# Kernel optimization log

Hardware: AMD Instinct MI355X
Metric: run time of the kernel (lower is better)

The kernel has to match this reference:

```python
import jax, jax.numpy as jnp
import numpy as np

B, S, H, D = 2, 2048, 16, 64  # batch, seq, heads, head_dim


def setup_inputs() -> dict:
    key = jax.random.key(0)
    kq, kk, kv = jax.random.split(key, 3)
    query = jax.random.normal(kq, (B, S, H, D), dtype=jnp.float32)
    key_l = jax.random.normal(kk, (B, S, H, D), dtype=jnp.float32)
    value = jax.random.normal(kv, (B, S, H, D), dtype=jnp.float32)
    # padding mask: all tokens valid
    attention_mask = jnp.ones((B, S), dtype=bool)
    # causal lower-triangular mask [1,1,S,S]
    causal_mask = jnp.tril(jnp.ones((S, S), dtype=bool))[None, None, :, :]
    return {"query": query, "key": key_l, "value": value,
            "attention_mask": attention_mask, "causal_mask": causal_mask}


def reference(query, key, value, attention_mask, causal_mask):
    b = query.shape[0]
    # broadcast causal mask to batch: (B,1,S,S)
    cm = jnp.broadcast_to(causal_mask, (b,) + causal_mask.shape[1:])
    # padding mask (B,S) -> (B,1,1,S), combine with causal
    am = attention_mask[:, None, None, :]
    mask = jnp.logical_and(cm, am)
    neg = jnp.finfo(query.dtype).min
    bias = jnp.where(mask, jnp.zeros((), query.dtype), jnp.full((), neg, query.dtype))
    sm_scale = 1.0 / jnp.sqrt(jnp.asarray(query.shape[-1], jnp.float32))
    # scores: (B,H,Sq,Sk)
    scores = jnp.einsum("bqhd,bkhd->bhqk", query, key) * sm_scale + bias
    # attention_softmax_in_fp32 = True
    probs = jax.nn.softmax(scores.astype(jnp.float32), axis=-1).astype(query.dtype)
    ctx = jnp.einsum("bhqk,bkhd->bqhd", probs, value)
    # merge heads -> hidden_size_per_partition
    return ctx.reshape(ctx.shape[0], ctx.shape[1], -1)
```

## Files before the change

kernel.cpp:

```cpp
#include <hip/hip_runtime.h>
#include <hip/hip_bf16.h>


typedef __attribute__((ext_vector_type(8))) short short8;
typedef __attribute__((ext_vector_type(4))) short short4v;
typedef __attribute__((ext_vector_type(4))) float f32x4;

__device__ __forceinline__ unsigned cvtpk(float a, float b) {
    __hip_bfloat162 h = __float22bfloat162_rn(make_float2(a, b));
    union { __hip_bfloat162 h; unsigned u; } c; c.h = h;
    return c.u;
}

__device__ __forceinline__ short8 pack8(float4 a, float4 b) {
    union { short8 s; unsigned u[4]; } w;
    w.u[0] = cvtpk(a.x, a.y); w.u[1] = cvtpk(a.z, a.w);
    w.u[2] = cvtpk(b.x, b.y); w.u[3] = cvtpk(b.z, b.w);
    return w.s;
}

__device__ __forceinline__ unsigned short f2b(float v) {
    union { __hip_bfloat16 h; unsigned short u; } c;
    c.h = __float2bfloat16(v);
    return c.u;
}

__device__ __forceinline__ float b2f(unsigned short u) {
    union { unsigned u; float f; } v; v.u = ((unsigned)u) << 16;
    return v.f;
}

#define TR64(dst, addr) \
    asm volatile("ds_read_b64_tr_b16 %0, %1" : "=v"(dst) : "v"(addr))

#define GLOAD_LDS16(g, l) \
    __builtin_amdgcn_global_load_lds((const __attribute__((address_space(1))) void*)(g), \
                                     (__attribute__((address_space(3))) void*)(l), 16, 0, 0)

__constant__ unsigned char JOBS[48][3] = {
    {31,0,16},{31,16,32},{30,15,31},{15,0,16},
    {30,0,15},{29,0,15},{29,15,30},{28,14,29},{14,0,15},
    {28,0,14},{27,0,14},{27,14,28},{26,13,27},{13,0,14},
    {26,0,13},{25,0,13},{25,13,26},{24,12,25},{12,0,13},
    {24,0,12},{23,0,12},{23,12,24},{22,11,23},{11,0,12},
    {22,0,11},{21,0,11},{21,11,22},{20,10,21},{10,0,11},
    {20,0,10},{19,0,10},{19,10,20},{18,9,19},{9,0,10},
    {18,0,9},{17,0,9},{17,9,18},{16,8,17},{8,0,9},
    {16,0,8},{7,0,8},
    {6,0,7},{5,0,6},{4,0,5},{3,0,4},{2,0,3},{1,0,2},{0,0,1}
};

__global__ __launch_bounds__(256, 4)
void CoreAttention_68710886801875_prepass(const float* __restrict__ K,
                                          const float* __restrict__ V,
                                          unsigned short* __restrict__ Kbf,
                                          unsigned short* __restrict__ Vbf)
{
    const int tile = blockIdx.x;
    const int bh = tile >> 5, kt = tile & 31;
    const size_t base = (size_t)(bh >> 4) * (2048 * 1024) + (size_t)(bh & 15) * 64;
    unsigned short* ktile = Kbf + (size_t)tile * 4096;
    unsigned short* vtile = Vbf + (size_t)tile * 4096;

#pragma unroll
    for (int it = 0; it < 2; ++it) {
        const int c = threadIdx.x + it * 256;
        {
            const int r  = c >> 3;
            const int c8 = (c & 7) ^ (r & 7);
            const float* src = K + base + (size_t)(kt * 64 + r) * 1024 + c8 * 8;
            *(short8*)(ktile + c * 8) = pack8(*(const float4*)src, *(const float4*)(src + 4));
        }
        {
            const int s = c >> 3, k_lo = (c >> 1) & 3, half = c & 1;
            const int k  = (s >> 2) * 4 + k_lo;
            const int c8 = (s & 3) * 2 + half;
            const float* src = V + base + (size_t)(kt * 64 + k) * 1024 + c8 * 8;
            *(short8*)(vtile + c * 8) = pack8(*(const float4*)src, *(const float4*)(src + 4));
        }
    }
}

template <int PRE>
__global__ __launch_bounds__(256, 4)
void CoreAttention_68710886801875_kernel(const float* __restrict__ Q,
                                         const float* __restrict__ K,
                                         const float* __restrict__ V,
                                         const unsigned short* __restrict__ Kbf,
                                         const unsigned short* __restrict__ Vbf,
                                         float* __restrict__ O,
                                         unsigned short* __restrict__ Opart,
                                         float* __restrict__ Lpart)
{
    constexpr int S = 2048, HD = 1024;
    constexpr float SCALE = 0.125f * 1.44269504088896340736f;

    __shared__ __align__(16) unsigned short ldsK[2][64 * 64];
    __shared__ __align__(16) unsigned short ldsV[2][64 * 64];
    __shared__ __align__(16) unsigned short ldsPT[4][64 * 16];

    const int tid = threadIdx.x;
    const int wid = tid >> 6, lane = tid & 63, g = lane >> 4, lm = lane & 15;

    const int bx     = blockIdx.x;
    const int r_     = bx >> 3;
    const int jobIdx = r_ >> 2;
    const int bh     = (bx & 7) * 4 + (r_ & 3);
    const int qt     = JOBS[jobIdx][0];
    const int t0     = JOBS[jobIdx][1];
    const int t1     = JOBS[jobIdx][2];
    const int b      = bh >> 4, h = bh & 15;
    const int q0     = qt << 6;
    const size_t base = ((size_t)b * S) * HD + (size_t)h * 64;

    const int r0 = tid >> 3, c8 = tid & 7;
    const float* kp0 = K + base + (size_t)r0 * HD + c8 * 8;
    const float* vp0 = V + base + (size_t)r0 * HD + c8 * 8;
    float4 kst[4], vst[4];
    const unsigned short* kbfB = Kbf + (size_t)bh * 32 * 4096;
    const unsigned short* vbfB = Vbf + (size_t)bh * 32 * 4096;

    auto STAGE_ISSUE = [&](int kt2, int buf) {
        if constexpr (PRE) {
            const unsigned short* ks = kbfB + (size_t)kt2 * 4096 + tid * 8;
            const unsigned short* vs = vbfB + (size_t)kt2 * 4096 + tid * 8;
            GLOAD_LDS16(ks,        &ldsK[buf][tid * 8]);
            GLOAD_LDS16(ks + 2048, &ldsK[buf][tid * 8 + 2048]);
            GLOAD_LDS16(vs,        &ldsV[buf][tid * 8]);
            GLOAD_LDS16(vs + 2048, &ldsV[buf][tid * 8 + 2048]);
        } else {
            const float* kp = kp0 + (size_t)kt2 * 64 * HD;
            const float* vp = vp0 + (size_t)kt2 * 64 * HD;
            kst[0] = *(const float4*)kp;
            kst[1] = *(const float4*)(kp + 4);
            kst[2] = *(const float4*)(kp + (size_t)32 * HD);
            kst[3] = *(const float4*)(kp + (size_t)32 * HD + 4);
            vst[0] = *(const float4*)vp;
            vst[1] = *(const float4*)(vp + 4);
            vst[2] = *(const float4*)(vp + (size_t)32 * HD);
            vst[3] = *(const float4*)(vp + (size_t)32 * HD + 4);
        }
    };
    auto STAGE_WRITE = [&](int buf) {
        if constexpr (!PRE) {
#pragma unroll
            for (int it = 0; it < 2; ++it) {
                const int r = r0 + it * 32;
                const unsigned byteK = (unsigned)((r * 128 + c8 * 16) ^ ((r & 7) << 4));
                *(short8*)((char*)&ldsK[buf][0] + byteK) = pack8(kst[it * 2], kst[it * 2 + 1]);
                const unsigned byteV = (unsigned)(((r >> 2) * 4 + (c8 >> 1)) * 128 +
                                                  (r & 3) * 32 + (c8 & 1) * 16);
                *(short8*)((char*)&ldsV[buf][0] + byteV) = pack8(vst[it * 2], vst[it * 2 + 1]);
            }
        }
    };

    short8 qf[2];
    {
        const float* qp = Q + base + (size_t)(q0 + wid * 16 + lm) * HD + g * 8;
#pragma unroll
        for (int ks = 0; ks < 2; ++ks) {
            float4 a = *(const float4*)(qp + ks * 32);
            float4 cc = *(const float4*)(qp + ks * 32 + 4);
            a.x *= SCALE; a.y *= SCALE; a.z *= SCALE; a.w *= SCALE;
            cc.x *= SCALE; cc.y *= SCALE; cc.z *= SCALE; cc.w *= SCALE;
            qf[ks] = pack8(a, cc);
        }
    }

    short8 ones;
#pragma unroll
    for (int j = 0; j < 8; ++j) ones[j] = (short)0x3F80;

    f32x4 oacc[4], lacc;
#pragma unroll
    for (int n = 0; n < 4; ++n) oacc[n] = (f32x4){0.f, 0.f, 0.f, 0.f};
    lacc = (f32x4){0.f, 0.f, 0.f, 0.f};

    const unsigned vBase = (unsigned)(size_t)&ldsV[0][0];
    const unsigned ptAddr = (unsigned)(size_t)&ldsPT[wid][0];

    STAGE_ISSUE(t0, 0);
    STAGE_WRITE(0);
    __syncthreads();

    for (int t = t0; t < t1; ++t) {
        const int cur = (t - t0) & 1;
        if (t + 1 < t1) STAGE_ISSUE(t + 1, cur ^ 1);

        const bool diag = (t == qt);
        const int nmax = diag ? wid : 3;

        f32x4 sv[4];
        __builtin_amdgcn_s_setprio(1);
#pragma unroll
        for (int n = 0; n < 4; ++n) {
            if (n <= nmax) {
                const int kr = n * 16 + lm;
                const unsigned b0 = cur * 8192u +
                    (unsigned)((kr * 128 + g * 16) ^ ((kr & 7) << 4));
                const unsigned b1 = cur * 8192u +
                    (unsigned)((kr * 128 + 64 + g * 16) ^ ((kr & 7) << 4));
                const short8 kf0 = *(const short8*)((const char*)&ldsK[0][0] + b0);
                const short8 kf1 = *(const short8*)((const char*)&ldsK[0][0] + b1);
                f32x4 acc = (f32x4){0.f, 0.f, 0.f, 0.f};
                acc = __builtin_amdgcn_mfma_f32_16x16x32_bf16(qf[0], kf0, acc, 0, 0, 0);
                acc = __builtin_amdgcn_mfma_f32_16x16x32_bf16(qf[1], kf1, acc, 0, 0, 0);
                if (diag && n == wid) {
#pragma unroll
                    for (int r = 0; r < 4; ++r)
                        if (lm > g * 4 + r) acc[r] = -1e30f;
                }
                sv[n] = acc;
            } else {
                sv[n] = (f32x4){-1e30f, -1e30f, -1e30f, -1e30f};
            }
        }
        __builtin_amdgcn_s_setprio(0);

#pragma unroll
        for (int n = 0; n < 4; ++n) {
            float p[4];
#pragma unroll
            for (int r = 0; r < 4; ++r) p[r] = exp2f(sv[n][r]);
            union { short4v s; unsigned uu[2]; } pk;
            pk.uu[0] = cvtpk(p[0], p[1]);
            pk.uu[1] = cvtpk(p[2], p[3]);
            const unsigned byte = (unsigned)((n * 4 + (lm >> 2)) * 128 +
                                             (lm & 3) * 32 + g * 8);
            *(short4v*)((char*)&ldsPT[wid][0] + byte) = pk.s;
        }

        asm volatile("s_waitcnt lgkmcnt(0)" ::: "memory");
        short4v vlo[2][4], vhi[2][4], pL[2], pH[2];
#pragma unroll
        for (int ks = 0; ks < 2; ++ks) {
            const unsigned sub = (unsigned)(8 * ks + 2 * g);
#pragma unroll
            for (int n = 0; n < 4; ++n) {
                const unsigned va = vBase + cur * 8192u + (sub * 4 + n) * 128 + lm * 8;
                TR64(vlo[ks][n], va);
                TR64(vhi[ks][n], va + 512);
            }
            const unsigned pa = ptAddr + sub * 128 + lm * 8;
            TR64(pL[ks], pa);
            TR64(pH[ks], pa + 128);
        }
        asm volatile("s_waitcnt lgkmcnt(0)" ::: "memory");
        __builtin_amdgcn_sched_barrier(0);
        __builtin_amdgcn_s_setprio(1);
#pragma unroll
        for (int ks = 0; ks < 2; ++ks) {
            const short8 pf = __builtin_shufflevector(pL[ks], pH[ks],
                                                      0, 1, 2, 3, 4, 5, 6, 7);
            lacc = __builtin_amdgcn_mfma_f32_16x16x32_bf16(pf, ones, lacc, 0, 0, 0);
#pragma unroll
            for (int n = 0; n < 4; ++n) {
                const short8 vf = __builtin_shufflevector(vlo[ks][n], vhi[ks][n],
                                                          0, 1, 2, 3, 4, 5, 6, 7);
                oacc[n] = __builtin_amdgcn_mfma_f32_16x16x32_bf16(pf, vf, oacc[n], 0, 0, 0);
            }
        }
        __builtin_amdgcn_s_setprio(0);

        if (t + 1 < t1) STAGE_WRITE(cur ^ 1);
        __syncthreads();
    }

    if (qt >= 16) {
        const int part = ((bh * 16 + (qt - 16)) << 1) + (t0 != 0 ? 1 : 0);
        unsigned short* op = Opart + (size_t)part * 4096;
        float* lp = Lpart + part * 64;
#pragma unroll
        for (int r = 0; r < 4; ++r) {
            const int row = wid * 16 + g * 4 + r;
            if (lm == 0) lp[row] = lacc[r];
#pragma unroll
            for (int n = 0; n < 4; ++n)
                op[row * 64 + n * 16 + lm] = f2b(oacc[n][r]);
        }
    } else {
#pragma unroll
        for (int r = 0; r < 4; ++r) {
            const float inv = 1.0f / lacc[r];
            const int row = q0 + wid * 16 + g * 4 + r;
            float* op = O + base + (size_t)row * HD;
#pragma unroll
            for (int n = 0; n < 4; ++n)
                op[n * 16 + lm] = oacc[n][r] * inv;
        }
    }
}

__global__ __launch_bounds__(256, 8)
void CoreAttention_68710886801875_combine(const unsigned short* __restrict__ Opart,
                                          const float* __restrict__ Lpart,
                                          float* __restrict__ O)
{
    const int sid = blockIdx.x;
    const int bh = sid >> 4, tt = sid & 15;
    const int qt = 16 + tt;
    const size_t base = (size_t)(bh >> 4) * (2048 * 1024) + (size_t)(bh & 15) * 64;
    const unsigned short* A = Opart + (size_t)sid * 2 * 4096;
    const unsigned short* Bp = A + 4096;
    const float* la = Lpart + sid * 2 * 64;
    const float* lb = la + 64;

    const int tid = threadIdx.x;
    const int r = tid >> 2;
    const int c0 = (tid & 3) * 16;
    const float inv = 1.0f / (la[r] + lb[r]);
    float* op = O + base + (size_t)(qt * 64 + r) * 1024;
#pragma unroll
    for (int j = 0; j < 16; ++j) {
        const int c = c0 + j;
        op[c] = (b2f(A[r * 64 + c]) + b2f(Bp[r * 64 + c])) * inv;
    }
}

extern "C" void kernel_launch(void* const* d_in, const int* in_sizes, int n_in,
                              void* d_out, int out_size, void* d_ws, size_t ws_size,
                              hipStream_t stream) {
    (void)in_sizes; (void)n_in; (void)out_size;
    const float* Q = (const float*)d_in[0];
    const float* K = (const float*)d_in[1];
    const float* V = (const float*)d_in[2];
    float* O = (float*)d_out;

    const size_t IMG    = 16777216ull;
    const size_t PART_O = 1024ull * 4096 * 2;
    const size_t PART_L = 1024ull * 64 * 4;

    if (ws_size >= IMG + PART_O + PART_L) {
        unsigned short* Kbf = (unsigned short*)d_ws;
        unsigned short* Vbf = Kbf + 4194304;
        unsigned short* Opart = (unsigned short*)((char*)d_ws + IMG);
        float* Lpart = (float*)((char*)d_ws + IMG + PART_O);
        hipLaunchKernelGGL(CoreAttention_68710886801875_prepass,
                           dim3(1024), dim3(256), 0, stream, K, V, Kbf, Vbf);
        hipLaunchKernelGGL((CoreAttention_68710886801875_kernel<1>),
                           dim3(1536), dim3(256), 0, stream, Q, K, V, Kbf, Vbf, O,
                           Opart, Lpart);
        hipLaunchKernelGGL(CoreAttention_68710886801875_combine,
                           dim3(512), dim3(256), 0, stream, Opart, Lpart, O);
    } else {
        unsigned short* Opart = (unsigned short*)d_ws;
        float* Lpart = (float*)((char*)d_ws + PART_O);
        hipLaunchKernelGGL((CoreAttention_68710886801875_kernel<0>),
                           dim3(1536), dim3(256), 0, stream, Q, K, V,
                           (const unsigned short*)nullptr, (const unsigned short*)nullptr,
                           O, Opart, Lpart);
        hipLaunchKernelGGL(CoreAttention_68710886801875_combine,
                           dim3(512), dim3(256), 0, stream, Opart, Lpart, O);
    }
}
```

Before: 66.24 us.

## Double query tile to 128 rows per block and rebalance causal job table

Each block now handles 128 query rows, with each wave computing two 16-row sub-tiles that share the same K/V fragments loaded from LDS. This halves the number of blocks and the K/V staging per query row. The job table is rebuilt for 16 query tiles with split-KV halves for the later tiles, and the combine kernel and workspace layout are resized to match. It also raises per-thread register use (launch bounds lowered to 3 blocks per CU), and waves skip KV tiles past their diagonal, so work within a block is uneven.

```diff
diff --git a/kernel.cpp b/kernel.cpp
--- a/kernel.cpp
+++ b/kernel.cpp
@@ -37,17 +37,10 @@
     __builtin_amdgcn_global_load_lds((const __attribute__((address_space(1))) void*)(g), \
                                      (__attribute__((address_space(3))) void*)(l), 16, 0, 0)
 
-__constant__ unsigned char JOBS[48][3] = {
-    {31,0,16},{31,16,32},{30,15,31},{15,0,16},
-    {30,0,15},{29,0,15},{29,15,30},{28,14,29},{14,0,15},
-    {28,0,14},{27,0,14},{27,14,28},{26,13,27},{13,0,14},
-    {26,0,13},{25,0,13},{25,13,26},{24,12,25},{12,0,13},
-    {24,0,12},{23,0,12},{23,12,24},{22,11,23},{11,0,12},
-    {22,0,11},{21,0,11},{21,11,22},{20,10,21},{10,0,11},
-    {20,0,10},{19,0,10},{19,10,20},{18,9,19},{9,0,10},
-    {18,0,9},{17,0,9},{17,9,18},{16,8,17},{8,0,9},
-    {16,0,8},{7,0,8},
-    {6,0,7},{5,0,6},{4,0,5},{3,0,4},{2,0,3},{1,0,2},{0,0,1}
+__constant__ unsigned char JOBS[24][3] = {
+    {15,0,16},{7,0,16},{14,0,15},{14,15,30},{13,14,28},{6,0,14},{12,13,26},{11,12,24},
+    {15,16,32},{13,0,14},{12,0,13},{10,0,11},{10,11,22},{9,0,10},{11,0,12},{5,0,12},
+    {0,0,2},{1,0,4},{2,0,6},{3,0,8},{8,0,9},{9,10,20},{8,9,18},{4,0,10}
 };
 
 __global__ __launch_bounds__(256, 4)
@@ -82,7 +75,7 @@
 }
 
 template <int PRE>
-__global__ __launch_bounds__(256, 4)
+__global__ __launch_bounds__(256, 3)
 void CoreAttention_68710886801875_kernel(const float* __restrict__ Q,
                                          const float* __restrict__ K,
                                          const float* __restrict__ V,
@@ -97,7 +90,7 @@
 
     __shared__ __align__(16) unsigned short ldsK[2][64 * 64];
     __shared__ __align__(16) unsigned short ldsV[2][64 * 64];
-    __shared__ __align__(16) unsigned short ldsPT[4][64 * 16];
+    __shared__ __align__(16) unsigned short ldsPT[4][2][64 * 16];
 
     const int tid = threadIdx.x;
     const int wid = tid >> 6, lane = tid & 63, g = lane >> 4, lm = lane & 15;
@@ -110,7 +103,9 @@
     const int t0     = JOBS[jobIdx][1];
     const int t1     = JOBS[jobIdx][2];
     const int b      = bh >> 4, h = bh & 15;
-    const int q0     = qt << 6;
+    const int q0     = qt << 7;
+    const int diagT  = 2 * qt + (wid >> 1);
+    const int nd     = (wid & 1) << 1;
     const size_t base = ((size_t)b * S) * HD + (size_t)h * 64;
 
     const int r0 = tid >> 3, c8 = tid & 7;
@@ -155,16 +150,17 @@
         }
     };
 
-    short8 qf[2];
-    {
-        const float* qp = Q + base + (size_t)(q0 + wid * 16 + lm) * HD + g * 8;
+    short8 qf[2][2];
+#pragma unroll
+    for (int m = 0; m < 2; ++m) {
+        const float* qp = Q + base + (size_t)(q0 + wid * 32 + m * 16 + lm) * HD + g * 8;
 #pragma unroll
         for (int ks = 0; ks < 2; ++ks) {
             float4 a = *(const float4*)(qp + ks * 32);
             float4 cc = *(const float4*)(qp + ks * 32 + 4);
             a.x *= SCALE; a.y *= SCALE; a.z *= SCALE; a.w *= SCALE;
             cc.x *= SCALE; cc.y *= SCALE; cc.z *= SCALE; cc.w *= SCALE;
-            qf[ks] = pack8(a, cc);
+            qf[m][ks] = pack8(a, cc);
         }
     }
 
@@ -172,13 +168,16 @@
 #pragma unroll
     for (int j = 0; j < 8; ++j) ones[j] = (short)0x3F80;
 
-    f32x4 oacc[4], lacc;
-#pragma unroll
-    for (int n = 0; n < 4; ++n) oacc[n] = (f32x4){0.f, 0.f, 0.f, 0.f};
-    lacc = (f32x4){0.f, 0.f, 0.f, 0.f};
+    f32x4 oacc[2][4], lacc[2];
+#pragma unroll
+    for (int m = 0; m < 2; ++m) {
+        lacc[m] = (f32x4){0.f, 0.f, 0.f, 0.f};
+#pragma unroll
+        for (int n = 0; n < 4; ++n) oacc[m][n] = (f32x4){0.f, 0.f, 0.f, 0.f};
+    }
 
     const unsigned vBase = (unsigned)(size_t)&ldsV[0][0];
-    const unsigned ptAddr = (unsigned)(size_t)&ldsPT[wid][0];
+    const unsigned ptAddr = (unsigned)(size_t)&ldsPT[wid][0][0];
 
     STAGE_ISSUE(t0, 0);
     STAGE_WRITE(0);
@@ -188,107 +187,126 @@
         const int cur = (t - t0) & 1;
         if (t + 1 < t1) STAGE_ISSUE(t + 1, cur ^ 1);
 
-        const bool diag = (t == qt);
-        const int nmax = diag ? wid : 3;
-
-        f32x4 sv[4];
-        __builtin_amdgcn_s_setprio(1);
-#pragma unroll
-        for (int n = 0; n < 4; ++n) {
-            if (n <= nmax) {
-                const int kr = n * 16 + lm;
-                const unsigned b0 = cur * 8192u +
-                    (unsigned)((kr * 128 + g * 16) ^ ((kr & 7) << 4));
-                const unsigned b1 = cur * 8192u +
-                    (unsigned)((kr * 128 + 64 + g * 16) ^ ((kr & 7) << 4));
-                const short8 kf0 = *(const short8*)((const char*)&ldsK[0][0] + b0);
-                const short8 kf1 = *(const short8*)((const char*)&ldsK[0][0] + b1);
-                f32x4 acc = (f32x4){0.f, 0.f, 0.f, 0.f};
-                acc = __builtin_amdgcn_mfma_f32_16x16x32_bf16(qf[0], kf0, acc, 0, 0, 0);
-                acc = __builtin_amdgcn_mfma_f32_16x16x32_bf16(qf[1], kf1, acc, 0, 0, 0);
-                if (diag && n == wid) {
-#pragma unroll
-                    for (int r = 0; r < 4; ++r)
-                        if (lm > g * 4 + r) acc[r] = -1e30f;
-                }
-                sv[n] = acc;
-            } else {
-                sv[n] = (f32x4){-1e30f, -1e30f, -1e30f, -1e30f};
-            }
-        }
-        __builtin_amdgcn_s_setprio(0);
-
-#pragma unroll
-        for (int n = 0; n < 4; ++n) {
-            float p[4];
-#pragma unroll
-            for (int r = 0; r < 4; ++r) p[r] = exp2f(sv[n][r]);
-            union { short4v s; unsigned uu[2]; } pk;
-            pk.uu[0] = cvtpk(p[0], p[1]);
-            pk.uu[1] = cvtpk(p[2], p[3]);
-            const unsigned byte = (unsigned)((n * 4 + (lm >> 2)) * 128 +
-                                             (lm & 3) * 32 + g * 8);
-            *(short4v*)((char*)&ldsPT[wid][0] + byte) = pk.s;
-        }
-
-        asm volatile("s_waitcnt lgkmcnt(0)" ::: "memory");
-        short4v vlo[2][4], vhi[2][4], pL[2], pH[2];
-#pragma unroll
-        for (int ks = 0; ks < 2; ++ks) {
-            const unsigned sub = (unsigned)(8 * ks + 2 * g);
+        if (t <= diagT) {
+            const bool full = (t < diagT);
+
+            f32x4 sv[2][4];
+            __builtin_amdgcn_s_setprio(1);
 #pragma unroll
             for (int n = 0; n < 4; ++n) {
-                const unsigned va = vBase + cur * 8192u + (sub * 4 + n) * 128 + lm * 8;
-                TR64(vlo[ks][n], va);
-                TR64(vhi[ks][n], va + 512);
-            }
-            const unsigned pa = ptAddr + sub * 128 + lm * 8;
-            TR64(pL[ks], pa);
-            TR64(pH[ks], pa + 128);
-        }
-        asm volatile("s_waitcnt lgkmcnt(0)" ::: "memory");
-        __builtin_amdgcn_sched_barrier(0);
-        __builtin_amdgcn_s_setprio(1);
-#pragma unroll
-        for (int ks = 0; ks < 2; ++ks) {
-            const short8 pf = __builtin_shufflevector(pL[ks], pH[ks],
-                                                      0, 1, 2, 3, 4, 5, 6, 7);
-            lacc = __builtin_amdgcn_mfma_f32_16x16x32_bf16(pf, ones, lacc, 0, 0, 0);
-#pragma unroll
-            for (int n = 0; n < 4; ++n) {
-                const short8 vf = __builtin_shufflevector(vlo[ks][n], vhi[ks][n],
-                                                          0, 1, 2, 3, 4, 5, 6, 7);
-                oacc[n] = __builtin_amdgcn_mfma_f32_16x16x32_bf16(pf, vf, oacc[n], 0, 0, 0);
-            }
-        }
-        __builtin_amdgcn_s_setprio(0);
+                short8 kf0, kf1;
+                if (full || n <= nd + 1) {
+                    const int kr = n * 16 + lm;
+                    const unsigned b0 = cur * 8192u +
+                        (unsigned)((kr * 128 + g * 16) ^ ((kr & 7) << 4));
+                    const unsigned b1 = cur * 8192u +
+                        (unsigned)((kr * 128 + 64 + g * 16) ^ ((kr & 7) << 4));
+                    kf0 = *(const short8*)((const char*)&ldsK[0][0] + b0);
+                    kf1 = *(const short8*)((const char*)&ldsK[0][0] + b1);
+                }
+#pragma unroll
+                for (int m = 0; m < 2; ++m) {
+                    if (full || n <= nd + m) {
+                        f32x4 acc = (f32x4){0.f, 0.f, 0.f, 0.f};
+                        acc = __builtin_amdgcn_mfma_f32_16x16x32_bf16(qf[m][0], kf0, acc, 0, 0, 0);
+                        acc = __builtin_amdgcn_mfma_f32_16x16x32_bf16(qf[m][1], kf1, acc, 0, 0, 0);
+                        if (!full && n == nd + m) {
+#pragma unroll
+                            for (int r = 0; r < 4; ++r)
+                                if (lm > g * 4 + r) acc[r] = -1e30f;
+                        }
+                        sv[m][n] = acc;
+                    } else {
+                        sv[m][n] = (f32x4){-1e30f, -1e30f, -1e30f, -1e30f};
+                    }
+                }
+            }
+            __builtin_amdgcn_s_setprio(0);
+
+#pragma unroll
+            for (int m = 0; m < 2; ++m)
+#pragma unroll
+                for (int n = 0; n < 4; ++n) {
+                    float p[4];
+#pragma unroll
+                    for (int r = 0; r < 4; ++r) p[r] = exp2f(sv[m][n][r]);
+                    union { short4v s; unsigned uu[2]; } pk;
+                    pk.uu[0] = cvtpk(p[0], p[1]);
+                    pk.uu[1] = cvtpk(p[2], p[3]);
+                    const unsigned byte = (unsigned)((n * 4 + (lm >> 2)) * 128 +
+                                                     (lm & 3) * 32 + g * 8);
+                    *(short4v*)((char*)&ldsPT[wid][m][0] + byte) = pk.s;
+                }
+
+            asm volatile("s_waitcnt lgkmcnt(0)" ::: "memory");
+            short4v vlo[2][4], vhi[2][4], pL[2][2], pH[2][2];
+#pragma unroll
+            for (int ks = 0; ks < 2; ++ks) {
+                const unsigned sub = (unsigned)(8 * ks + 2 * g);
+#pragma unroll
+                for (int n = 0; n < 4; ++n) {
+                    const unsigned va = vBase + cur * 8192u + (sub * 4 + n) * 128 + lm * 8;
+                    TR64(vlo[ks][n], va);
+                    TR64(vhi[ks][n], va + 512);
+                }
+#pragma unroll
+                for (int m = 0; m < 2; ++m) {
+                    const unsigned pa = ptAddr + m * 2048u + sub * 128 + lm * 8;
+                    TR64(pL[m][ks], pa);
+                    TR64(pH[m][ks], pa + 128);
+                }
+            }
+            asm volatile("s_waitcnt lgkmcnt(0)" ::: "memory");
+            __builtin_amdgcn_sched_barrier(0);
+            __builtin_amdgcn_s_setprio(1);
+#pragma unroll
+            for (int m = 0; m < 2; ++m)
+#pragma unroll
+                for (int ks = 0; ks < 2; ++ks) {
+                    const short8 pf = __builtin_shufflevector(pL[m][ks], pH[m][ks],
+                                                              0, 1, 2, 3, 4, 5, 6, 7);
+                    lacc[m] = __builtin_amdgcn_mfma_f32_16x16x32_bf16(pf, ones, lacc[m], 0, 0, 0);
+#pragma unroll
+                    for (int n = 0; n < 4; ++n) {
+                        const short8 vf = __builtin_shufflevector(vlo[ks][n], vhi[ks][n],
+                                                                  0, 1, 2, 3, 4, 5, 6, 7);
+                        oacc[m][n] = __builtin_amdgcn_mfma_f32_16x16x32_bf16(pf, vf,
+                                                                             oacc[m][n], 0, 0, 0);
+                    }
+                }
+            __builtin_amdgcn_s_setprio(0);
+        }
 
         if (t + 1 < t1) STAGE_WRITE(cur ^ 1);
         __syncthreads();
     }
 
-    if (qt >= 16) {
-        const int part = ((bh * 16 + (qt - 16)) << 1) + (t0 != 0 ? 1 : 0);
-        unsigned short* op = Opart + (size_t)part * 4096;
-        float* lp = Lpart + part * 64;
-#pragma unroll
-        for (int r = 0; r < 4; ++r) {
-            const int row = wid * 16 + g * 4 + r;
-            if (lm == 0) lp[row] = lacc[r];
-#pragma unroll
-            for (int n = 0; n < 4; ++n)
-                op[row * 64 + n * 16 + lm] = f2b(oacc[n][r]);
-        }
+    if (qt >= 8) {
+        const int part = ((bh * 8 + (qt - 8)) << 1) + (t0 != 0 ? 1 : 0);
+        unsigned short* op = Opart + (size_t)part * 8192;
+        float* lp = Lpart + part * 128;
+#pragma unroll
+        for (int m = 0; m < 2; ++m)
+#pragma unroll
+            for (int r = 0; r < 4; ++r) {
+                const int row = wid * 32 + m * 16 + g * 4 + r;
+                if (lm == 0) lp[row] = lacc[m][r];
+#pragma unroll
+                for (int n = 0; n < 4; ++n)
+                    op[row * 64 + n * 16 + lm] = f2b(oacc[m][n][r]);
+            }
     } else {
 #pragma unroll
-        for (int r = 0; r < 4; ++r) {
-            const float inv = 1.0f / lacc[r];
-            const int row = q0 + wid * 16 + g * 4 + r;
-            float* op = O + base + (size_t)row * HD;
-#pragma unroll
-            for (int n = 0; n < 4; ++n)
-                op[n * 16 + lm] = oacc[n][r] * inv;
-        }
+        for (int m = 0; m < 2; ++m)
+#pragma unroll
+            for (int r = 0; r < 4; ++r) {
+                const float inv = 1.0f / lacc[m][r];
+                const int row = q0 + wid * 32 + m * 16 + g * 4 + r;
+                float* op = O + base + (size_t)row * HD;
+#pragma unroll
+                for (int n = 0; n < 4; ++n)
+                    op[n * 16 + lm] = oacc[m][n][r] * inv;
+            }
     }
 }
 
@@ -298,21 +316,20 @@
                                           float* __restrict__ O)
 {
     const int sid = blockIdx.x;
-    const int bh = sid >> 4, tt = sid & 15;
-    const int qt = 16 + tt;
+    const int bh = sid >> 3, qt = 8 + (sid & 7);
     const size_t base = (size_t)(bh >> 4) * (2048 * 1024) + (size_t)(bh & 15) * 64;
-    const unsigned short* A = Opart + (size_t)sid * 2 * 4096;
-    const unsigned short* Bp = A + 4096;
-    const float* la = Lpart + sid * 2 * 64;
-    const float* lb = la + 64;
+    const unsigned short* A = Opart + (size_t)sid * 2 * 8192;
+    const unsigned short* Bp = A + 8192;
+    const float* la = Lpart + sid * 2 * 128;
+    const float* lb = la + 128;
 
     const int tid = threadIdx.x;
-    const int r = tid >> 2;
-    const int c0 = (tid & 3) * 16;
+    const int r = tid >> 1;
+    const int c0 = (tid & 1) * 32;
     const float inv = 1.0f / (la[r] + lb[r]);
-    float* op = O + base + (size_t)(qt * 64 + r) * 1024;
-#pragma unroll
-    for (int j = 0; j < 16; ++j) {
+    float* op = O + base + (size_t)(qt * 128 + r) * 1024;
+#pragma unroll
+    for (int j = 0; j < 32; ++j) {
         const int c = c0 + j;
         op[c] = (b2f(A[r * 64 + c]) + b2f(Bp[r * 64 + c])) * inv;
     }
@@ -328,8 +345,8 @@
     float* O = (float*)d_out;
 
     const size_t IMG    = 16777216ull;
-    const size_t PART_O = 1024ull * 4096 * 2;
-    const size_t PART_L = 1024ull * 64 * 4;
+    const size_t PART_O = 512ull * 8192 * 2;
+    const size_t PART_L = 512ull * 128 * 4;
 
     if (ws_size >= IMG + PART_O + PART_L) {
         unsigned short* Kbf = (unsigned short*)d_ws;
@@ -339,18 +356,18 @@
         hipLaunchKernelGGL(CoreAttention_68710886801875_prepass,
                            dim3(1024), dim3(256), 0, stream, K, V, Kbf, Vbf);
         hipLaunchKernelGGL((CoreAttention_68710886801875_kernel<1>),
-                           dim3(1536), dim3(256), 0, stream, Q, K, V, Kbf, Vbf, O,
+                           dim3(768), dim3(256), 0, stream, Q, K, V, Kbf, Vbf, O,
                            Opart, Lpart);
         hipLaunchKernelGGL(CoreAttention_68710886801875_combine,
-                           dim3(512), dim3(256), 0, stream, Opart, Lpart, O);
+                           dim3(256), dim3(256), 0, stream, Opart, Lpart, O);
     } else {
         unsigned short* Opart = (unsigned short*)d_ws;
         float* Lpart = (float*)((char*)d_ws + PART_O);
         hipLaunchKernelGGL((CoreAttention_68710886801875_kernel<0>),
-                           dim3(1536), dim3(256), 0, stream, Q, K, V,
+                           dim3(768), dim3(256), 0, stream, Q, K, V,
                            (const unsigned short*)nullptr, (const unsigned short*)nullptr,
                            O, Opart, Lpart);
         hipLaunchKernelGGL(CoreAttention_68710886801875_combine,
-                           dim3(512), dim3(256), 0, stream, Opart, Lpart, O);
-    }
-}
+                           dim3(256), dim3(256), 0, stream, Opart, Lpart, O);
+    }
+}
```

Result: faster. 62.59 us, median of 2 (-5.5%).
